# Performance work log

Hardware: AMD Instinct MI355X
Metric: run time of the kernel (lower is better)

## Reference

```python
import jax, jax.numpy as jnp
import numpy as np

jax.config.update("jax_enable_x64", True)  # faithful int64 LIF state, as in the torch module

NUM_INPUTS = 700
NUM_HIDDEN = 4096
NUM_OUTPUT = 20
N_STEPS = 1000
ALPHA_SHIFT = 4   # synaptic-current decay shift
BETA_SHIFT = 3    # membrane decay shift
THRESHOLD = 1
BW1 = 64
BW2 = 64


def _sat(x, bw):
    # Quantize.saturate + to_int: clamp to signed bw-bit range, cast to int64.
    lo = -(2 ** (bw - 1))
    hi = 2 ** (bw - 1) - 1
    if jnp.issubdtype(x.dtype, jnp.floating):
        # values here are far below 2**63, so the float clip/cast is exact
        return jnp.clip(x, float(lo), float(hi)).astype(jnp.int64)
    return jnp.clip(x, lo, hi)


def _decay(v, shift):
    # LIF.exp_decay: v - (v >> shift) with arithmetic right shift on int64
    return v - (v >> shift)


def setup_inputs() -> dict:
    key = jax.random.key(0)
    k1, k2, k3, k4 = jax.random.split(key, 4)
    input_spikes = jax.random.randint(k1, (N_STEPS, NUM_INPUTS), 0, 2, dtype=jnp.int64)
    w1 = jax.random.randint(k2, (NUM_HIDDEN, NUM_INPUTS), -8, 8, dtype=jnp.int64)
    v1 = jax.random.randint(k3, (NUM_HIDDEN, NUM_HIDDEN), -8, 8, dtype=jnp.int64)
    w2 = jax.random.randint(k4, (NUM_OUTPUT, NUM_HIDDEN), -8, 8, dtype=jnp.int64)
    return {"input_spikes": input_spikes, "w1": w1, "v1": v1, "w2": w2}


def reference(input_spikes, w1, v1, w2):
    w1f = w1.astype(jnp.float32)
    v1f = v1.astype(jnp.float32)
    w2f = w2.astype(jnp.float32)
    # feed-forward input currents for all timesteps at once: [T, H]
    in_all = _sat(jnp.einsum("hi,ti->th", w1f, input_spikes.astype(jnp.float32)), BW1)

    H = w1.shape[0]
    O = w2.shape[0]
    z = lambda n: jnp.zeros((n,), dtype=jnp.int64)
    # state: hidden spikes, hidden mem, hidden syn, readout mem, readout syn
    init = (z(H), z(H), z(H), z(O), z(O))

    def step(state, in_cur):
        h_out, h_mem, h_syn, r_mem, r_syn = state
        # recurrent feedback current from PREVIOUS step's hidden spikes
        fb = _sat(jnp.einsum("hk,k->h", v1f, h_out.astype(jnp.float32)), BW1)
        syn_curr = _sat(in_cur + fb, BW1)
        # hidden LIF: reset (by previous spike) -> threshold -> decay/integrate
        h_mem = jnp.where(h_out == 1, 0, h_mem)
        new_out = (h_mem - THRESHOLD > 0).astype(jnp.int64)
        new_mem = _decay(h_mem, BETA_SHIFT) + h_syn
        new_syn = _decay(h_syn, ALPHA_SHIFT) + syn_curr
        # readout LIF (no reset); records updated membrane
        ro_cur = _sat(jnp.einsum("oh,h->o", w2f, new_out.astype(jnp.float32)), BW2)
        new_rmem = _decay(r_mem, BETA_SHIFT) + r_syn
        new_rsyn = _decay(r_syn, ALPHA_SHIFT) + ro_cur
        return (new_out, new_mem, new_syn, new_rmem, new_rsyn), new_rmem

    _, rec = jax.lax.scan(step, init, in_all)  # rec: [T, O]
    return rec.T  # torch.stack(ro_mem_rec, dim=1) -> [num_output, n_steps]
```

## Files before the change

kernel.cpp:

```cpp
#include <hip/hip_runtime.h>

#define T_STEPS 1000
#define N_IN    700
#define N_HID   4096
#define N_OUT   20
#define NBLK    256
#define NPB     16

typedef unsigned int u32x4 __attribute__((ext_vector_type(4)));
typedef unsigned int u32x2 __attribute__((ext_vector_type(2)));

__device__ __forceinline__ unsigned load_rec4(const unsigned* p) {
    unsigned r;
    asm volatile("global_load_dword %0, %1, off sc0 sc1\n\t"
                 "s_waitcnt vmcnt(0)"
                 : "=v"(r) : "v"(p) : "memory");
    return r;
}
__device__ __forceinline__ void store_rec4(unsigned* p, unsigned v) {
    asm volatile("global_store_dword %0, %1, off sc0 sc1"
                 :: "v"(p), "v"(v) : "memory");
}

__global__ __launch_bounds__(256) void k_transpose_i8(
    const int* __restrict__ in, signed char* __restrict__ out,
    int R, int C, int out_stride)
{
    __shared__ signed char tile[32][33];
    const int cx = blockIdx.x * 32;
    const int ry = blockIdx.y * 32;
    const int tx = threadIdx.x;
    const int ty = threadIdx.y;
#pragma unroll
    for (int r = 0; r < 4; ++r) {
        int row = ry + ty + r * 8;
        int col = cx + tx;
        if (row < R && col < C)
            tile[ty + r * 8][tx] = (signed char)in[(size_t)row * C + col];
    }
    __syncthreads();
#pragma unroll
    for (int r = 0; r < 4; ++r) {
        int c   = cx + ty + r * 8;
        int row = ry + tx;
        if (c < C && row < R)
            out[(size_t)c * out_stride + row] = tile[tx][ty + r * 8];
    }
}

__global__ __launch_bounds__(256) void k_prep_v1n(
    const int* __restrict__ in, unsigned char* __restrict__ out)
{
    __shared__ unsigned char tile[16][64];
    const int k0 = blockIdx.x * 64;
    const int b  = blockIdx.y;
    const int t  = threadIdx.x;
    const int kk = t & 63;
#pragma unroll
    for (int r = 0; r < 4; ++r) {
        int hl = (t >> 6) + r * 4;
        tile[hl][kk] = (unsigned char)(in[(size_t)(b * NPB + hl) * N_HID + k0 + kk] + 8);
    }
    __syncthreads();
    if (t < 64) {
        unsigned w0 = 0, w1 = 0;
#pragma unroll
        for (int j = 0; j < 8; ++j) w0 |= (unsigned)tile[j][t] << (4 * j);
#pragma unroll
        for (int j = 0; j < 8; ++j) w1 |= (unsigned)tile[8 + j][t] << (4 * j);
        u32x2 v = {w0, w1};
        *(u32x2*)(out + ((size_t)b << 15) + ((size_t)(k0 + t) << 3)) = v;
    }
}

__global__ __launch_bounds__(256) void k_inall(
    const signed char* __restrict__ w1t,
    const int* __restrict__ spk,
    short* __restrict__ in_all2)
{
    __shared__ int s_spk[16][N_IN];
    const int t0 = blockIdx.y * 16;
    const int tcnt = min(16, T_STEPS - t0);
    const int tid = threadIdx.x;
    for (int b = 0; b < tcnt; ++b)
        for (int i = tid; i < N_IN; i += 256)
            s_spk[b][i] = spk[(size_t)(t0 + b) * N_IN + i];
    __syncthreads();
    const int h = blockIdx.x * 256 + tid;
    int acc[16];
#pragma unroll
    for (int b = 0; b < 16; ++b) acc[b] = 0;
    for (int i = 0; i < N_IN; ++i) {
        int w = (int)w1t[(size_t)i * N_HID + h];
#pragma unroll
        for (int b = 0; b < 16; ++b) acc[b] += w * s_spk[b][i];
    }
    const size_t base = (size_t)(h >> 4) * (T_STEPS * NPB) + (h & 15);
    for (int b = 0; b < tcnt; ++b)
        in_all2[base + (size_t)(t0 + b) * NPB] = (short)acc[b];
}

__global__ __launch_bounds__(64) void k_main(
    const short* __restrict__ in_all2,
    const u32x2* __restrict__ v1n,
    unsigned* __restrict__ pub)
{
    const int lane = threadIdx.x;
    const int bid  = blockIdx.x;
    const int j    = lane & 15;

    __shared__ u32x2 s_w[N_HID + 1];
    __shared__ u32x4 s_rec[2][64];

    {
        const u32x2* src = v1n + ((size_t)bid << 12);
        for (int r = lane; r < N_HID; r += 64) s_w[r] = src[r];
        if (lane == 0) { u32x2 z = {0u, 0u}; s_w[N_HID] = z; }
    }
    asm volatile("s_waitcnt vmcnt(0) lgkmcnt(0)" ::: "memory");

    if (lane == 0) store_rec4(pub + bid, 0x10000u);

    int mm = 0, synv = 0, out_t = 0;
    const short* in_base = in_all2 + (size_t)bid * (T_STEPS * NPB) + j;
    const u32x2* wl = s_w + (lane << 6);
    const int bz = N_HID - (lane << 6);
    const unsigned M4 = 0x0F0F0F0Fu, M8 = 0x00FF00FFu;
    const int j0 = j & 1, j1 = j & 2, j3 = j & 8;

    for (int t = 0; t < T_STEPS; ++t) {
        const int cur = t & 1;
        asm volatile("s_waitcnt vmcnt(0)" ::: "memory");
        __builtin_amdgcn_sched_barrier(0);

        int mem_t = (mm - (mm >> 3)) + synv;
        int mnext = out_t ? 0 : mem_t;
        int out_n = (mnext - 1 > 0) ? 1 : 0;
        unsigned om = (unsigned)__ballot(out_n) & 0xFFFFu;
        if (lane == 0) store_rec4(pub + (size_t)(t + 1) * NBLK + bid, 0x10000u | om);
        mm = mnext; out_t = out_n;

        int in_cur = (int)in_base[t * NPB];

        __builtin_amdgcn_global_load_lds(
            (const void*)(pub + (size_t)t * NBLK + (lane << 2)),
            (void*)&s_rec[cur ^ 1][0], 16, 0,  17);

        unsigned mlo = 0, mhi = 0;
        if (t > 0) {
            u32x4 q = s_rec[cur][lane];
            if (((q.x & q.y & q.z & q.w) & 0x10000u) == 0u) {
                const unsigned* rp = pub + (size_t)(t - 1) * NBLK + (lane << 2);
                while (!(q.x & 0x10000u)) { __builtin_amdgcn_s_sleep(1); q.x = load_rec4(rp + 0); }
                while (!(q.y & 0x10000u)) { __builtin_amdgcn_s_sleep(1); q.y = load_rec4(rp + 1); }
                while (!(q.z & 0x10000u)) { __builtin_amdgcn_s_sleep(1); q.z = load_rec4(rp + 2); }
                while (!(q.w & 0x10000u)) { __builtin_amdgcn_s_sleep(1); q.w = load_rec4(rp + 3); }
            }
            mlo = (q.x & 0xFFFFu) | ((q.y & 0xFFFFu) << 16);
            mhi = (q.z & 0xFFFFu) | ((q.w & 0xFFFFu) << 16);
        }
        unsigned long long m = ((unsigned long long)mhi << 32) | mlo;
        int myc = __popcll(m);

        unsigned a0=0,a1=0,a2=0,a3=0,a4=0,a5=0,a6=0,a7=0;
        while (__any((int)(m != 0ull))) {
            unsigned be0=0, bo0=0, be1=0, bo1=0;
#pragma unroll
            for (int u = 0; u < 16; ++u) {
                int b = m ? (int)__builtin_ctzll(m) : bz;
                m &= m - 1;
                u32x2 w = wl[b];
                be0 += w.x & M4;  bo0 += (w.x >> 4) & M4;
                be1 += w.y & M4;  bo1 += (w.y >> 4) & M4;
            }
            a0 += be0 & M8;  a1 += (be0 >> 8) & M8;
            a2 += bo0 & M8;  a3 += (bo0 >> 8) & M8;
            a4 += be1 & M8;  a5 += (be1 >> 8) & M8;
            a6 += bo1 & M8;  a7 += (bo1 >> 8) & M8;
        }

        unsigned e0 = (j0 ? a2 : a0) + __shfl_xor(j0 ? a0 : a2, 1);
        unsigned e1 = (j0 ? a3 : a1) + __shfl_xor(j0 ? a1 : a3, 1);
        unsigned e2 = (j0 ? a6 : a4) + __shfl_xor(j0 ? a4 : a6, 1);
        unsigned e3 = (j0 ? a7 : a5) + __shfl_xor(j0 ? a5 : a7, 1);
        unsigned f0 = (j1 ? e1 : e0) + __shfl_xor(j1 ? e0 : e1, 2);
        unsigned f1 = (j1 ? e3 : e2) + __shfl_xor(j1 ? e2 : e3, 2);
        unsigned g  = (j3 ? f1 : f0) + __shfl_xor(j3 ? f0 : f1, 8);
        g += __shfl_xor(g, 4);
        g += __shfl_xor(g, 16);
        g += __shfl_xor(g, 32);
        myc += __shfl_xor(myc, 1);  myc += __shfl_xor(myc, 2);
        myc += __shfl_xor(myc, 4);  myc += __shfl_xor(myc, 8);
        myc += __shfl_xor(myc, 16); myc += __shfl_xor(myc, 32);

        int field = (int)((g >> ((j & 4) << 2)) & 0xFFFFu);
        int fb = field - 8 * myc;

        synv = (synv - (synv >> 4)) + in_cur + fb;
    }
}

__global__ __launch_bounds__(256) void k_rocur(
    const int* __restrict__ w2,
    const unsigned* __restrict__ pub,
    int* __restrict__ ro)
{
    const int t = blockIdx.x;
    const int tid = threadIdx.x;
    __shared__ unsigned short s_list[N_HID];
    __shared__ int s_red[32][8];
    __shared__ int s_n;
    if (tid < 64) {
        const unsigned* rp = pub + (size_t)t * NBLK + (tid << 2);
        unsigned long long m =
            (unsigned long long)((rp[0] & 0xFFFFu) | ((rp[1] & 0xFFFFu) << 16)) |
            ((unsigned long long)((rp[2] & 0xFFFFu) | ((rp[3] & 0xFFFFu) << 16)) << 32);
        int cnt = __popcll(m);
        int inc = cnt;
#pragma unroll
        for (int d = 1; d < 64; d <<= 1) {
            int v = __shfl_up(inc, d);
            if (tid >= d) inc += v;
        }
        int p = inc - cnt;
        while (m) {
            s_list[p++] = (unsigned short)((tid << 6) | __builtin_ctzll(m));
            m &= m - 1;
        }
        if (tid == 63) s_n = inc;
    }
    __syncthreads();
    const int n = s_n;
    const int o = tid >> 3;
    const int r = tid & 7;
    if (o < N_OUT) {
        int acc = 0;
        for (int jj = r; jj < n; jj += 8) acc += w2[(size_t)o * N_HID + s_list[jj]];
        s_red[o][r] = acc;
    }
    __syncthreads();
    if (tid < N_OUT) {
        int acc = 0;
#pragma unroll
        for (int q = 0; q < 8; ++q) acc += s_red[tid][q];
        ro[(size_t)t * N_OUT + tid] = acc;
    }
}

#define CH 250
__global__ __launch_bounds__(256) void k_scan(const int* __restrict__ ro,
                                              int* __restrict__ out)
{
    __shared__ int s_ro[CH * N_OUT];
    __shared__ int s_out[CH * N_OUT];
    const int tid = threadIdx.x;
    int rm = 0, rs = 0;
    for (int c = 0; c < T_STEPS / CH; ++c) {
        for (int i = tid; i < CH * N_OUT; i += 256)
            s_ro[i] = ro[c * CH * N_OUT + i];
        __syncthreads();
        if (tid < N_OUT) {
            for (int jj = 0; jj < CH; ++jj) {
                rm = (rm - (rm >> 3)) + rs;
                rs = (rs - (rs >> 4)) + s_ro[jj * N_OUT + tid];
                s_out[jj * N_OUT + tid] = rm;
            }
        }
        __syncthreads();
        for (int i = tid; i < CH * N_OUT; i += 256) {
            int o = i / CH, jj = i - o * CH;
            out[o * T_STEPS + c * CH + jj] = s_out[jj * N_OUT + o];
        }
        __syncthreads();
    }
}

extern "C" void kernel_launch(void* const* d_in, const int* in_sizes, int n_in,
                              void* d_out, int out_size, void* d_ws, size_t ws_size,
                              hipStream_t stream)
{
    const int* spk = (const int*)d_in[0];
    const int* w1  = (const int*)d_in[1];
    const int* v1  = (const int*)d_in[2];
    const int* w2  = (const int*)d_in[3];
    int* out = (int*)d_out;

    char* ws = (char*)d_ws;
    constexpr size_t SZ_PUB    = (size_t)(T_STEPS + 1) * NBLK * 4;
    constexpr size_t OFF_PUB   = 0;
    constexpr size_t OFF_INALL = OFF_PUB + SZ_PUB;
    constexpr size_t OFF_V1N   = OFF_INALL + 8192000;
    constexpr size_t OFF_W1T   = OFF_V1N + 8388608;
    constexpr size_t OFF_RO    = OFF_W1T + 2867200;

    unsigned*       pub    = (unsigned*)(ws + OFF_PUB);
    short*          in_all = (short*)(ws + OFF_INALL);
    unsigned char*  v1n    = (unsigned char*)(ws + OFF_V1N);
    signed char*    w1t    = (signed char*)(ws + OFF_W1T);
    int*            ro     = (int*)(ws + OFF_RO);

    hipMemsetAsync(pub, 0, SZ_PUB, stream);

    dim3 tb(32, 8);
    k_prep_v1n<<<dim3(64, 256), 256, 0, stream>>>(v1, v1n);
    k_transpose_i8<<<dim3(22, 128), tb, 0, stream>>>(w1, w1t, N_HID, N_IN, N_HID);
    k_inall<<<dim3(16, 63), 256, 0, stream>>>(w1t, spk, in_all);

    k_main<<<dim3(NBLK), dim3(64), 0, stream>>>(in_all, (const u32x2*)v1n, pub);

    k_rocur<<<dim3(T_STEPS), 256, 0, stream>>>(w2, pub, ro);
    k_scan<<<1, 256, 0, stream>>>(ro, out);
}
```

Before: 1.952 ms.

## Process two timesteps per sync iteration in recurrent LIF kernel

```diff
diff --git a/kernel.cpp b/kernel.cpp
--- a/kernel.cpp
+++ b/kernel.cpp
@@ -10,9 +10,9 @@
 typedef unsigned int u32x4 __attribute__((ext_vector_type(4)));
 typedef unsigned int u32x2 __attribute__((ext_vector_type(2)));
 
-__device__ __forceinline__ unsigned load_rec4(const unsigned* p) {
-    unsigned r;
-    asm volatile("global_load_dword %0, %1, off sc0 sc1\n\t"
+__device__ __forceinline__ u32x4 load_rec_syncx4(const u32x4* p) {
+    u32x4 r;
+    asm volatile("global_load_dwordx4 %0, %1, off sc0 sc1\n\t"
                  "s_waitcnt vmcnt(0)"
                  : "=v"(r) : "v"(p) : "memory");
     return r;
@@ -95,9 +95,11 @@
 #pragma unroll
         for (int b = 0; b < 16; ++b) acc[b] += w * s_spk[b][i];
     }
-    const size_t base = (size_t)(h >> 4) * (T_STEPS * NPB) + (h & 15);
-    for (int b = 0; b < tcnt; ++b)
-        in_all2[base + (size_t)(t0 + b) * NPB] = (short)acc[b];
+    const size_t base = (size_t)(h >> 4) * (T_STEPS * NPB) + (size_t)(h & 15) * 2;
+    for (int b = 0; b < tcnt; ++b) {
+        int t = t0 + b;
+        in_all2[base + (size_t)(t >> 1) * 32 + (t & 1)] = (short)acc[b];
+    }
 }
 
 __global__ __launch_bounds__(64) void k_main(
@@ -110,7 +112,8 @@
     const int j    = lane & 15;
 
     __shared__ u32x2 s_w[N_HID + 1];
-    __shared__ u32x4 s_rec[2][64];
+    __shared__ u32x4 s_recA[2][64];
+    __shared__ u32x4 s_recB[2][64];
 
     {
         const u32x2* src = v1n + ((size_t)bid << 12);
@@ -121,83 +124,165 @@
 
     if (lane == 0) store_rec4(pub + bid, 0x10000u);
 
-    int mm = 0, synv = 0, out_t = 0;
-    const short* in_base = in_all2 + (size_t)bid * (T_STEPS * NPB) + j;
     const u32x2* wl = s_w + (lane << 6);
     const int bz = N_HID - (lane << 6);
     const unsigned M4 = 0x0F0F0F0Fu, M8 = 0x00FF00FFu;
     const int j0 = j & 1, j1 = j & 2, j3 = j & 8;
-
-    for (int t = 0; t < T_STEPS; ++t) {
-        const int cur = t & 1;
+    const int jsh = (j & 4) << 2;
+    const int* ip_base = (const int*)in_all2 + (size_t)bid * 8000 + j;
+
+#define BFLY_FIELD(a0,a1,a2,a3,a4,a5,a6,a7,gout) do {                      \
+        unsigned e0 = (j0 ? a2 : a0) + __shfl_xor(j0 ? a0 : a2, 1);        \
+        unsigned e1 = (j0 ? a3 : a1) + __shfl_xor(j0 ? a1 : a3, 1);        \
+        unsigned e2 = (j0 ? a6 : a4) + __shfl_xor(j0 ? a4 : a6, 1);        \
+        unsigned e3 = (j0 ? a7 : a5) + __shfl_xor(j0 ? a5 : a7, 1);        \
+        unsigned f0 = (j1 ? e1 : e0) + __shfl_xor(j1 ? e0 : e1, 2);        \
+        unsigned f1 = (j1 ? e3 : e2) + __shfl_xor(j1 ? e2 : e3, 2);        \
+        unsigned g  = (j3 ? f1 : f0) + __shfl_xor(j3 ? f0 : f1, 8);        \
+        g += __shfl_xor(g, 4); g += __shfl_xor(g, 16); g += __shfl_xor(g, 32); \
+        gout = g; } while (0)
+
+    int syn_m2 = 0;
+    int in1_prev = 0;
+    int mpr = 0;
+    int out_c = 0;
+    int nBred = 0;
+    unsigned bB0=0,bB1=0,bB2=0,bB3=0,bB4=0,bB5=0,bB6=0,bB7=0;
+    int ip_cur = ip_base[0];
+
+    for (int I = 0; I < T_STEPS / 2; ++I) {
+        const int cur = I & 1;
+
+        unsigned gBf;
+        BFLY_FIELD(bB0,bB1,bB2,bB3,bB4,bB5,bB6,bB7,gBf);
+        int fbB = (int)((gBf >> jsh) & 0xFFFFu) - 8 * nBred;
+        int syn_m1 = (syn_m2 - (syn_m2 >> 4)) + in1_prev + fbB;
+        int memv = (mpr - (mpr >> 3)) + syn_m1;
+        int mpr1 = out_c ? 0 : memv;
+        int out1 = (mpr1 - 1 > 0) ? 1 : 0;
+        unsigned om1 = (unsigned)__ballot(out1) & 0xFFFFu;
+
         asm volatile("s_waitcnt vmcnt(0)" ::: "memory");
         __builtin_amdgcn_sched_barrier(0);
 
-        int mem_t = (mm - (mm >> 3)) + synv;
-        int mnext = out_t ? 0 : mem_t;
-        int out_n = (mnext - 1 > 0) ? 1 : 0;
-        unsigned om = (unsigned)__ballot(out_n) & 0xFFFFu;
-        if (lane == 0) store_rec4(pub + (size_t)(t + 1) * NBLK + bid, 0x10000u | om);
-        mm = mnext; out_t = out_n;
-
-        int in_cur = (int)in_base[t * NPB];
+        if (lane == 0)
+            store_rec4(pub + (size_t)(2 * I + 1) * NBLK + bid, 0x10000u | om1);
+
+        unsigned mAlo = 0, mAhi = 0, mBlo = 0, mBhi = 0;
+        if (I > 0) {
+            u32x4 qA = s_recA[cur][lane];
+            if (((qA.x & qA.y & qA.z & qA.w) & 0x10000u) == 0u) {
+                const u32x4* rp = (const u32x4*)(pub + (size_t)(2 * I - 1) * NBLK) + lane;
+                do { __builtin_amdgcn_s_sleep(1); qA = load_rec_syncx4(rp); }
+                while (((qA.x & qA.y & qA.z & qA.w) & 0x10000u) == 0u);
+            }
+            u32x4 qB = s_recB[cur][lane];
+            if (((qB.x & qB.y & qB.z & qB.w) & 0x10000u) == 0u) {
+                const u32x4* rp = (const u32x4*)(pub + (size_t)(2 * I) * NBLK) + lane;
+                do { __builtin_amdgcn_s_sleep(1); qB = load_rec_syncx4(rp); }
+                while (((qB.x & qB.y & qB.z & qB.w) & 0x10000u) == 0u);
+            }
+            mAlo = (qA.x & 0xFFFFu) | ((qA.y & 0xFFFFu) << 16);
+            mAhi = (qA.z & 0xFFFFu) | ((qA.w & 0xFFFFu) << 16);
+            mBlo = (qB.x & 0xFFFFu) | ((qB.y & 0xFFFFu) << 16);
+            mBhi = (qB.z & 0xFFFFu) | ((qB.w & 0xFFFFu) << 16);
+        }
+        unsigned cnt = (unsigned)(__popc(mAlo) + __popc(mAhi))
+                     | ((unsigned)(__popc(mBlo) + __popc(mBhi)) << 16);
+        cnt += __shfl_xor(cnt, 1);  cnt += __shfl_xor(cnt, 2);
+        cnt += __shfl_xor(cnt, 4);  cnt += __shfl_xor(cnt, 8);
+        cnt += __shfl_xor(cnt, 16); cnt += __shfl_xor(cnt, 32);
+
+        int in0 = (ip_cur << 16) >> 16;
+        int in1 = ip_cur >> 16;
+
+        unsigned aA0=0,aA1=0,aA2=0,aA3=0,aA4=0,aA5=0,aA6=0,aA7=0;
+        unsigned gB0=0,gB1=0,gB2=0,gB3=0,gB4=0,gB5=0,gB6=0,gB7=0;
+        {
+            unsigned alo = mAlo, ahi = mAhi, blo = mBlo, bhi = mBhi;
+#pragma unroll
+            for (int grp = 0; grp < 2; ++grp) {
+                unsigned beA0=0,boA0=0,beA1=0,boA1=0;
+                unsigned beB0=0,boB0=0,beB1=0,boB1=0;
+#pragma unroll
+                for (int u = 0; u < 8; ++u) {
+                    int bA0 = alo ? (int)__builtin_ctz(alo) : bz;
+                    int bA1 = ahi ? (int)(32 + __builtin_ctz(ahi)) : bz;
+                    int bB0i = blo ? (int)__builtin_ctz(blo) : bz;
+                    int bB1i = bhi ? (int)(32 + __builtin_ctz(bhi)) : bz;
+                    alo &= alo - 1; ahi &= ahi - 1; blo &= blo - 1; bhi &= bhi - 1;
+                    u32x2 wA0 = wl[bA0], wA1 = wl[bA1];
+                    u32x2 wB0 = wl[bB0i], wB1 = wl[bB1i];
+                    beA0 += wA0.x & M4;  boA0 += (wA0.x >> 4) & M4;
+                    beA1 += wA0.y & M4;  boA1 += (wA0.y >> 4) & M4;
+                    beA0 += wA1.x & M4;  boA0 += (wA1.x >> 4) & M4;
+                    beA1 += wA1.y & M4;  boA1 += (wA1.y >> 4) & M4;
+                    beB0 += wB0.x & M4;  boB0 += (wB0.x >> 4) & M4;
+                    beB1 += wB0.y & M4;  boB1 += (wB0.y >> 4) & M4;
+                    beB0 += wB1.x & M4;  boB0 += (wB1.x >> 4) & M4;
+                    beB1 += wB1.y & M4;  boB1 += (wB1.y >> 4) & M4;
+                }
+                aA0 += beA0 & M8; aA1 += (beA0 >> 8) & M8;
+                aA2 += boA0 & M8; aA3 += (boA0 >> 8) & M8;
+                aA4 += beA1 & M8; aA5 += (beA1 >> 8) & M8;
+                aA6 += boA1 & M8; aA7 += (boA1 >> 8) & M8;
+                gB0 += beB0 & M8; gB1 += (beB0 >> 8) & M8;
+                gB2 += boB0 & M8; gB3 += (boB0 >> 8) & M8;
+                gB4 += beB1 & M8; gB5 += (beB1 >> 8) & M8;
+                gB6 += boB1 & M8; gB7 += (boB1 >> 8) & M8;
+            }
+            while (alo | ahi | blo | bhi) {
+                int bA0 = alo ? (int)__builtin_ctz(alo) : bz;
+                int bA1 = ahi ? (int)(32 + __builtin_ctz(ahi)) : bz;
+                int bB0i = blo ? (int)__builtin_ctz(blo) : bz;
+                int bB1i = bhi ? (int)(32 + __builtin_ctz(bhi)) : bz;
+                alo &= alo - 1; ahi &= ahi - 1; blo &= blo - 1; bhi &= bhi - 1;
+                u32x2 wA0 = wl[bA0], wA1 = wl[bA1];
+                u32x2 wB0 = wl[bB0i], wB1 = wl[bB1i];
+                unsigned beA0 = (wA0.x & M4) + (wA1.x & M4);
+                unsigned boA0 = ((wA0.x >> 4) & M4) + ((wA1.x >> 4) & M4);
+                unsigned beA1 = (wA0.y & M4) + (wA1.y & M4);
+                unsigned boA1 = ((wA0.y >> 4) & M4) + ((wA1.y >> 4) & M4);
+                unsigned beB0 = (wB0.x & M4) + (wB1.x & M4);
+                unsigned boB0 = ((wB0.x >> 4) & M4) + ((wB1.x >> 4) & M4);
+                unsigned beB1 = (wB0.y & M4) + (wB1.y & M4);
+                unsigned boB1 = ((wB0.y >> 4) & M4) + ((wB1.y >> 4) & M4);
+                aA0 += beA0 & M8; aA1 += (beA0 >> 8) & M8;
+                aA2 += boA0 & M8; aA3 += (boA0 >> 8) & M8;
+                aA4 += beA1 & M8; aA5 += (beA1 >> 8) & M8;
+                aA6 += boA1 & M8; aA7 += (boA1 >> 8) & M8;
+                gB0 += beB0 & M8; gB1 += (beB0 >> 8) & M8;
+                gB2 += boB0 & M8; gB3 += (boB0 >> 8) & M8;
+                gB4 += beB1 & M8; gB5 += (beB1 >> 8) & M8;
+                gB6 += boB1 & M8; gB7 += (boB1 >> 8) & M8;
+            }
+        }
+
+        unsigned gAf;
+        BFLY_FIELD(aA0,aA1,aA2,aA3,aA4,aA5,aA6,aA7,gAf);
+        int fbA = (int)((gAf >> jsh) & 0xFFFFu) - 8 * (int)(cnt & 0xFFFFu);
+        int syn0 = (syn_m1 - (syn_m1 >> 4)) + in0 + fbA;
+        int mem1 = (mpr1 - (mpr1 >> 3)) + syn0;
+        int mpr2 = out1 ? 0 : mem1;
+        int out2 = (mpr2 - 1 > 0) ? 1 : 0;
+        unsigned om2 = (unsigned)__ballot(out2) & 0xFFFFu;
+        if (lane == 0)
+            store_rec4(pub + (size_t)(2 * I + 2) * NBLK + bid, 0x10000u | om2);
 
         __builtin_amdgcn_global_load_lds(
-            (const void*)(pub + (size_t)t * NBLK + (lane << 2)),
-            (void*)&s_rec[cur ^ 1][0], 16, 0,  17);
-
-        unsigned mlo = 0, mhi = 0;
-        if (t > 0) {
-            u32x4 q = s_rec[cur][lane];
-            if (((q.x & q.y & q.z & q.w) & 0x10000u) == 0u) {
-                const unsigned* rp = pub + (size_t)(t - 1) * NBLK + (lane << 2);
-                while (!(q.x & 0x10000u)) { __builtin_amdgcn_s_sleep(1); q.x = load_rec4(rp + 0); }
-                while (!(q.y & 0x10000u)) { __builtin_amdgcn_s_sleep(1); q.y = load_rec4(rp + 1); }
-                while (!(q.z & 0x10000u)) { __builtin_amdgcn_s_sleep(1); q.z = load_rec4(rp + 2); }
-                while (!(q.w & 0x10000u)) { __builtin_amdgcn_s_sleep(1); q.w = load_rec4(rp + 3); }
-            }
-            mlo = (q.x & 0xFFFFu) | ((q.y & 0xFFFFu) << 16);
-            mhi = (q.z & 0xFFFFu) | ((q.w & 0xFFFFu) << 16);
-        }
-        unsigned long long m = ((unsigned long long)mhi << 32) | mlo;
-        int myc = __popcll(m);
-
-        unsigned a0=0,a1=0,a2=0,a3=0,a4=0,a5=0,a6=0,a7=0;
-        while (__any((int)(m != 0ull))) {
-            unsigned be0=0, bo0=0, be1=0, bo1=0;
-#pragma unroll
-            for (int u = 0; u < 16; ++u) {
-                int b = m ? (int)__builtin_ctzll(m) : bz;
-                m &= m - 1;
-                u32x2 w = wl[b];
-                be0 += w.x & M4;  bo0 += (w.x >> 4) & M4;
-                be1 += w.y & M4;  bo1 += (w.y >> 4) & M4;
-            }
-            a0 += be0 & M8;  a1 += (be0 >> 8) & M8;
-            a2 += bo0 & M8;  a3 += (bo0 >> 8) & M8;
-            a4 += be1 & M8;  a5 += (be1 >> 8) & M8;
-            a6 += bo1 & M8;  a7 += (bo1 >> 8) & M8;
-        }
-
-        unsigned e0 = (j0 ? a2 : a0) + __shfl_xor(j0 ? a0 : a2, 1);
-        unsigned e1 = (j0 ? a3 : a1) + __shfl_xor(j0 ? a1 : a3, 1);
-        unsigned e2 = (j0 ? a6 : a4) + __shfl_xor(j0 ? a4 : a6, 1);
-        unsigned e3 = (j0 ? a7 : a5) + __shfl_xor(j0 ? a5 : a7, 1);
-        unsigned f0 = (j1 ? e1 : e0) + __shfl_xor(j1 ? e0 : e1, 2);
-        unsigned f1 = (j1 ? e3 : e2) + __shfl_xor(j1 ? e2 : e3, 2);
-        unsigned g  = (j3 ? f1 : f0) + __shfl_xor(j3 ? f0 : f1, 8);
-        g += __shfl_xor(g, 4);
-        g += __shfl_xor(g, 16);
-        g += __shfl_xor(g, 32);
-        myc += __shfl_xor(myc, 1);  myc += __shfl_xor(myc, 2);
-        myc += __shfl_xor(myc, 4);  myc += __shfl_xor(myc, 8);
-        myc += __shfl_xor(myc, 16); myc += __shfl_xor(myc, 32);
-
-        int field = (int)((g >> ((j & 4) << 2)) & 0xFFFFu);
-        int fb = field - 8 * myc;
-
-        synv = (synv - (synv >> 4)) + in_cur + fb;
-    }
+            (const void*)(pub + (size_t)(2 * I + 1) * NBLK + (lane << 2)),
+            (void*)&s_recA[cur ^ 1][0], 16, 0, 17);
+        __builtin_amdgcn_global_load_lds(
+            (const void*)(pub + (size_t)(2 * I + 2) * NBLK + (lane << 2)),
+            (void*)&s_recB[cur ^ 1][0], 16, 0, 17);
+        int ip_next = ip_base[(I + 1) * 16];
+
+        syn_m2 = syn0; in1_prev = in1; mpr = mpr2; out_c = out2;
+        nBred = (int)(cnt >> 16);
+        bB0=gB0; bB1=gB1; bB2=gB2; bB3=gB3; bB4=gB4; bB5=gB5; bB6=gB6; bB7=gB7;
+        ip_cur = ip_next;
+    }
+#undef BFLY_FIELD
 }
 
 __global__ __launch_bounds__(256) void k_rocur(
@@ -286,7 +371,7 @@
     int* out = (int*)d_out;
 
     char* ws = (char*)d_ws;
-    constexpr size_t SZ_PUB    = (size_t)(T_STEPS + 1) * NBLK * 4;
+    constexpr size_t SZ_PUB    = (size_t)(T_STEPS + 4) * NBLK * 4;
     constexpr size_t OFF_PUB   = 0;
     constexpr size_t OFF_INALL = OFF_PUB + SZ_PUB;
     constexpr size_t OFF_V1N   = OFF_INALL + 8192000;
```

Result: slower. 3.130 ms (+60.4%).
